# Optimization experiments

Hardware: AMD Instinct MI355X
Metric: run time of the kernel (lower is better)

## Reference

```python
import jax, jax.numpy as jnp
import numpy as np

N, C_DEC, H, W = 16, 512, 32, 32
C_ENC, S, FEATS_IN, N_HEAD = 768, 77, 512, 8
EPS = 1e-5


def setup_inputs() -> dict:
    key = jax.random.key(0)
    ks = jax.random.split(key, 12)
    inp = {
        "input": jax.random.normal(ks[0], (N, C_DEC, H, W), jnp.float32),
        "cond": jax.random.normal(ks[1], (N, FEATS_IN), jnp.float32),
        "enc_hidden": jax.random.normal(ks[2], (N, S, C_ENC), jnp.float32),
        "enc_padding_mask": jax.random.randint(ks[3], (N, S), 0, 2).astype(jnp.float32),
        # AdaGN linear: feats_in -> 2*c_dec (scales, shifts)
        "adagn_w": jax.random.normal(ks[4], (2 * C_DEC, FEATS_IN), jnp.float32) * 0.02,
        "adagn_b": jnp.zeros((2 * C_DEC,), jnp.float32),
        # LayerNorm(c_enc) affine
        "ln_w": jnp.ones((C_ENC,), jnp.float32),
        "ln_b": jnp.zeros((C_ENC,), jnp.float32),
        # 1x1 conv q projection (treated as channel matmul)
        "q_w": jax.random.normal(ks[5], (C_DEC, C_DEC), jnp.float32) * 0.02,
        "q_b": jnp.zeros((C_DEC,), jnp.float32),
        # kv linear: c_enc -> 2*c_dec
        "kv_w": jax.random.normal(ks[6], (2 * C_DEC, C_ENC), jnp.float32) * 0.02,
        "kv_b": jnp.zeros((2 * C_DEC,), jnp.float32),
        # 1x1 conv out projection
        "out_w": jax.random.normal(ks[7], (C_DEC, C_DEC), jnp.float32) * 0.02,
        "out_b": jnp.zeros((C_DEC,), jnp.float32),
    }
    return inp


def reference(input, cond, enc_hidden, enc_padding_mask,
              adagn_w, adagn_b, ln_w, ln_b,
              q_w, q_b, kv_w, kv_b, out_w, out_b):
    n, c, h, w = input.shape
    d = c // N_HEAD

    # --- AdaGN: GroupNorm(1, c, affine=False) then cond-dependent scale/shift ---
    mu = jnp.mean(input, axis=(1, 2, 3), keepdims=True)
    var = jnp.var(input, axis=(1, 2, 3), keepdims=True)
    normed = (input - mu) * jax.lax.rsqrt(var + EPS)
    ss = cond @ adagn_w.T + adagn_b                      # [n, 2c]
    scales, shifts = ss[:, :c], ss[:, c:]
    x = shifts[:, :, None, None] + normed * (scales[:, :, None, None] + 1.0)

    # --- q projection (1x1 conv == per-pixel channel matmul) ---
    q = jnp.einsum('nchw,oc->nohw', x, q_w) + q_b[None, :, None, None]
    q = q.reshape(n, N_HEAD, d, h * w).transpose(0, 1, 3, 2)   # [n, head, hw, d]

    # --- encoder LayerNorm + kv projection ---
    mu_e = jnp.mean(enc_hidden, axis=-1, keepdims=True)
    var_e = jnp.var(enc_hidden, axis=-1, keepdims=True)
    e = (enc_hidden - mu_e) * jax.lax.rsqrt(var_e + EPS) * ln_w + ln_b
    kv = e @ kv_w.T + kv_b                               # [n, S, 2c]
    s = kv.shape[1]
    kv = kv.reshape(n, s, 2 * N_HEAD, d).transpose(0, 2, 1, 3)  # [n, 2*head, S, d]
    k, v = kv[:, :N_HEAD], kv[:, N_HEAD:]

    # --- scaled dot-product attention with additive padding mask ---
    scale = d ** (-0.25)
    att = jnp.einsum('nhqd,nhkd->nhqk', q * scale, k * scale)
    att = att - enc_padding_mask[:, None, None, :] * 10000.0
    att = jax.nn.softmax(att, axis=-1)
    y = jnp.einsum('nhqk,nhkd->nhqd', att, v)            # [n, head, hw, d]
    y = y.transpose(0, 1, 3, 2).reshape(n, c, h, w)

    out = jnp.einsum('nchw,oc->nohw', y, out_w) + out_b[None, :, None, None]
    return input + out
```

## Files before the change

### kernel.cpp

```cpp
#include <hip/hip_runtime.h>
#include <math.h>

typedef unsigned short u16;
typedef __bf16 bf16x8 __attribute__((ext_vector_type(8)));
typedef float f32x4 __attribute__((ext_vector_type(4)));

#define AS1 __attribute__((address_space(1)))
#define AS3 __attribute__((address_space(3)))

#define N_    16
#define C_    512
#define HW_   1024
#define CE_   768
#define S_    77
#define NH_   8
#define D_    64
#define FEATS_ 512
#define EPS_  1e-5f
#define TOK_  (N_ * S_)

#define WS_PSTAT 0
#define WS_QBIAS 1024
#define WSU_BYTE 131072
#define U_QW  0
#define U_OW  262144
#define U_KVW 524288
#define U_EB  1310720
#define U_KVB 2256896
#define U_QT  3518464
#define U_XT  11907072

__device__ __forceinline__ u16 f2bf(float f) {
    unsigned u = __float_as_uint(f);
    return (u16)((u + 0x7FFFu + ((u >> 16) & 1u)) >> 16);
}

__global__ __launch_bounds__(256) void mega1_kernel(const float* __restrict__ inp,
                                                    float* __restrict__ pstats,
                                                    const float* __restrict__ qw,
                                                    const float* __restrict__ ow,
                                                    const float* __restrict__ kvw,
                                                    u16* __restrict__ uq,
                                                    u16* __restrict__ uo,
                                                    u16* __restrict__ ukv,
                                                    const float* __restrict__ enc,
                                                    const float* __restrict__ lnw,
                                                    const float* __restrict__ lnb,
                                                    u16* __restrict__ eb,
                                                    const float* __restrict__ cond,
                                                    const float* __restrict__ agw,
                                                    const float* __restrict__ agb,
                                                    float* __restrict__ ssf) {
    __shared__ __align__(16) float smem[16384];
    int bid = blockIdx.x;
    int tid = threadIdx.x;
    if (bid < 256) {
        int n = bid >> 4, slice = bid & 15;
        const float* base = inp + (size_t)n * C_ * HW_ + slice * (C_ * HW_ / 16);
        float s = 0.f, s2 = 0.f;
        const float4* b4 = (const float4*)base;
        for (int i = tid; i < (C_ * HW_ / 16) / 4; i += 256) {
            float4 v = b4[i];
            s  += v.x + v.y + v.z + v.w;
            s2 += v.x * v.x + v.y * v.y + v.z * v.z + v.w * v.w;
        }
        for (int off = 32; off; off >>= 1) {
            s  += __shfl_down(s, off);
            s2 += __shfl_down(s2, off);
        }
        int wid = tid >> 6, lane = tid & 63;
        if (lane == 0) { smem[wid] = s; smem[4 + wid] = s2; }
        __syncthreads();
        if (tid == 0) {
            pstats[bid * 2]     = smem[0] + smem[1] + smem[2] + smem[3];
            pstats[bid * 2 + 1] = smem[4] + smem[5] + smem[6] + smem[7];
        }
    } else if (bid < 1536) {
        int i = (bid - 256) * 256 + tid;
        const float* s; u16* d; int j;
        if (i < 65536)       { s = qw;  d = uq;  j = i; }
        else if (i < 131072) { s = ow;  d = uo;  j = i - 65536; }
        else                 { s = kvw; d = ukv; j = i - 131072; }
        float4 v = ((const float4*)s)[j];
        ushort4 w;
        w.x = f2bf(v.x); w.y = f2bf(v.y); w.z = f2bf(v.z); w.w = f2bf(v.w);
        ((ushort4*)(d))[j] = w;
    } else if (bid < 2768) {
        int tok = bid - 1536;
        const float* row = enc + (size_t)tok * CE_;
        int t = tid;
        float v0 = row[t], v1 = row[t + 256], v2 = row[t + 512];
        float sum = v0 + v1 + v2;
        float sq  = v0 * v0 + v1 * v1 + v2 * v2;
        for (int off = 32; off; off >>= 1) {
            sum += __shfl_down(sum, off);
            sq  += __shfl_down(sq, off);
        }
        int wid = t >> 6, lane = t & 63;
        if (lane == 0) { smem[wid] = sum; smem[4 + wid] = sq; }
        __syncthreads();
        float tot = smem[0] + smem[1] + smem[2] + smem[3];
        float tsq = smem[4] + smem[5] + smem[6] + smem[7];
        float mu  = tot / CE_;
        float var = tsq / CE_ - mu * mu;
        float rstd = rsqrtf(var + EPS_);
        u16* o = eb + (size_t)tok * CE_;
        o[t]       = f2bf((v0 - mu) * rstd * lnw[t] + lnb[t]);
        o[t + 256] = f2bf((v1 - mu) * rstd * lnw[t + 256] + lnb[t + 256]);
        o[t + 512] = f2bf((v2 - mu) * rstd * lnw[t + 512] + lnb[t + 512]);
    } else {
        float (*wz)[512] = (float(*)[512])smem;
        float (*cz)[512] = (float(*)[512])(smem + 8192);
        int r0 = (bid - 2768) * 16;
        for (int i = tid; i < 2048; i += 256) {
            int row = i >> 7, f4 = i & 127;
            *(float4*)&cz[row][f4 * 4] = ((const float4*)(cond + (size_t)row * 512))[f4];
            *(float4*)&wz[row][f4 * 4] = ((const float4*)(agw + (size_t)(r0 + row) * 512))[f4];
        }
        __syncthreads();
        int n = tid >> 4, r = tid & 15;
        float acc = agb[r0 + r];
        for (int i = 0; i < 128; i++) {
            int j = (r + i) & 127;
            float4 c4 = *(const float4*)&cz[n][j * 4];
            float4 w4 = *(const float4*)&wz[r][j * 4];
            acc += c4.x * w4.x + c4.y * w4.y + c4.z * w4.z + c4.w * w4.w;
        }
        ssf[(size_t)n * 1024 + r0 + r] = acc;
    }
}

__global__ __launch_bounds__(256) void mega2_kernel(const float* __restrict__ inp,
                                                    const float* __restrict__ ssf,
                                                    const float* __restrict__ pstats,
                                                    u16* __restrict__ xT,
                                                    const float* __restrict__ qw,
                                                    const float* __restrict__ qb,
                                                    float* __restrict__ qbias) {
    __shared__ __align__(16) float smem[16384];
    __shared__ float muS[16], rsS[16];
    int bid = blockIdx.x;
    int tid = threadIdx.x;
    float cnt = (float)(C_ * HW_);
    if (bid < 2048) {
        int n = bid >> 7, rem = bid & 127;
        int c0 = (rem >> 4) * 64, h0 = (rem & 15) * 64;
        float s = 0.f, s2 = 0.f;
        for (int k = 0; k < 16; k++) {
            s  += pstats[(n * 16 + k) * 2];
            s2 += pstats[(n * 16 + k) * 2 + 1];
        }
        float mu = s / cnt;
        float rstd = rsqrtf(s2 / cnt - mu * mu + EPS_);
        float (*t)[65] = (float(*)[65])smem;
        int rr = tid >> 4, cc = (tid & 15) * 4;
#pragma unroll
        for (int i = 0; i < 4; i++) {
            int cl = rr + i * 16;
            int c = c0 + cl;
            float a = rstd * (ssf[(size_t)n * 1024 + c] + 1.f);
            float4 v = *(const float4*)(inp + ((size_t)n * C_ + c) * HW_ + h0 + cc);
            t[cl][cc + 0] = v.x * a; t[cl][cc + 1] = v.y * a;
            t[cl][cc + 2] = v.z * a; t[cl][cc + 3] = v.w * a;
        }
        __syncthreads();
#pragma unroll
        for (int i = 0; i < 4; i++) {
            int hl = rr + i * 16;
            ushort4 w;
            w.x = f2bf(t[cc + 0][hl]); w.y = f2bf(t[cc + 1][hl]);
            w.z = f2bf(t[cc + 2][hl]); w.w = f2bf(t[cc + 3][hl]);
            *(ushort4*)(xT + ((size_t)n * HW_ + h0 + hl) * C_ + c0 + cc) = w;
        }
    } else {
        float (*wz)[512] = (float(*)[512])smem;
        float (*cz)[512] = (float(*)[512])(smem + 8192);
        int r0 = (bid - 2048) * 16;
        if (tid < 16) {
            float s = 0.f, s2 = 0.f;
            for (int k = 0; k < 16; k++) {
                s  += pstats[(tid * 16 + k) * 2];
                s2 += pstats[(tid * 16 + k) * 2 + 1];
            }
            float mu = s / cnt;
            muS[tid] = mu;
            rsS[tid] = rsqrtf(s2 / cnt - mu * mu + EPS_);
        }
        __syncthreads();
        for (int i = tid; i < 2048; i += 256) {
            int row = i >> 7, f4 = i & 127;
            float4 sc4 = ((const float4*)(ssf + (size_t)row * 1024))[f4];
            float4 sh4 = ((const float4*)(ssf + (size_t)row * 1024 + 512))[f4];
            float mu = muS[row], rs = rsS[row];
            float4 b;
            b.x = sh4.x - mu * (rs * (sc4.x + 1.f));
            b.y = sh4.y - mu * (rs * (sc4.y + 1.f));
            b.z = sh4.z - mu * (rs * (sc4.z + 1.f));
            b.w = sh4.w - mu * (rs * (sc4.w + 1.f));
            *(float4*)&cz[row][f4 * 4] = b;
            *(float4*)&wz[row][f4 * 4] = ((const float4*)(qw + (size_t)(r0 + row) * 512))[f4];
        }
        __syncthreads();
        int n = tid >> 4, r = tid & 15;
        float acc = qb[r0 + r];
        for (int i = 0; i < 128; i++) {
            int j = (r + i) & 127;
            float4 c4 = *(const float4*)&cz[n][j * 4];
            float4 w4 = *(const float4*)&wz[r][j * 4];
            acc += c4.x * w4.x + c4.y * w4.y + c4.z * w4.z + c4.w * w4.w;
        }
        qbias[(size_t)n * 512 + r0 + r] = acc;
    }
}

__device__ __forceinline__ void gemm_mainloop(const u16* __restrict__ A, int lda, int arow0,
                                              const u16* __restrict__ B, int ldb, int brow0, int brmax,
                                              int K, f32x4 (&acc)[4][4], u16* As, u16* Bs) {
    int tid = threadIdx.x;
    int lane = tid & 63;
    int wm = ((tid >> 6) >> 1) * 64, wn = ((tid >> 6) & 1) * 64;
    int srow = tid >> 3;
    int sw = (tid & 7) ^ (srow & 7);
    int ldsoff = tid * 8;
    for (int kt = 0; kt < K; kt += 64) {
        __syncthreads();
#pragma unroll
        for (int i = 0; i < 4; i++) {
            int ar = arow0 + i * 32 + srow;
            const u16* ga = A + (size_t)ar * lda + kt + sw * 8;
            __builtin_amdgcn_global_load_lds((AS1 void*)ga, (AS3 void*)(As + i * 2048 + ldsoff), 16, 0, 0);
            int br = brow0 + i * 32 + srow; if (br > brmax) br = brmax;
            const u16* gb = B + (size_t)br * ldb + kt + sw * 8;
            __builtin_amdgcn_global_load_lds((AS1 void*)gb, (AS3 void*)(Bs + i * 2048 + ldsoff), 16, 0, 0);
        }
        __syncthreads();
#pragma unroll
        for (int kk = 0; kk < 2; kk++) {
            bf16x8 af[4], bfv[4];
            int ks = kk * 4 + (lane >> 4);
#pragma unroll
            for (int mi = 0; mi < 4; mi++) {
                int r = wm + mi * 16 + (lane & 15);
                af[mi] = *(const bf16x8*)(As + r * 64 + (ks ^ (r & 7)) * 8);
            }
#pragma unroll
            for (int ni = 0; ni < 4; ni++) {
                int r = wn + ni * 16 + (lane & 15);
                bfv[ni] = *(const bf16x8*)(Bs + r * 64 + (ks ^ (r & 7)) * 8);
            }
#pragma unroll
            for (int mi = 0; mi < 4; mi++)
#pragma unroll
                for (int ni = 0; ni < 4; ni++)
                    acc[mi][ni] = __builtin_amdgcn_mfma_f32_16x16x32_bf16(af[mi], bfv[ni], acc[mi][ni], 0, 0, 0);
        }
    }
}

__global__ __launch_bounds__(256) void mega3_kernel(const u16* __restrict__ qwb,
                                                    const u16* __restrict__ xT,
                                                    const float* __restrict__ qbias,
                                                    u16* __restrict__ qt,
                                                    const u16* __restrict__ kvwb,
                                                    const u16* __restrict__ eb,
                                                    const float* __restrict__ kvbias,
                                                    u16* __restrict__ kvo) {
    __shared__ __align__(16) u16 As[128 * 64];
    __shared__ __align__(16) u16 Bs[128 * 64];
    int bid = blockIdx.x;
    int lane = threadIdx.x & 63, wid = threadIdx.x >> 6;
    int wm = (wid >> 1) * 64, wn = (wid & 1) * 64;
    f32x4 acc[4][4];
#pragma unroll
    for (int mi = 0; mi < 4; mi++)
#pragma unroll
        for (int ni = 0; ni < 4; ni++) acc[mi][ni] = 0.f;

    if (bid < 512) {
        int n = bid >> 5, r = bid & 31;
        int brow0 = (r & 7) * 128, arow0 = (r >> 3) * 128;
        gemm_mainloop(qwb, C_, arow0, xT + (size_t)n * HW_ * C_, C_, brow0, HW_ - 1, C_, acc, As, Bs);
        u16* CT = qt + (size_t)n * HW_ * C_;
        const float* qbn = qbias + n * C_;
#pragma unroll
        for (int mi = 0; mi < 4; mi++) {
            int row = arow0 + wm + mi * 16 + ((lane >> 4) << 2);
            float4 b4 = *(const float4*)(qbn + row);
#pragma unroll
            for (int ni = 0; ni < 4; ni++) {
                int col = brow0 + wn + ni * 16 + (lane & 15);
                f32x4 v = acc[mi][ni];
                ushort4 w;
                w.x = f2bf(v.x + b4.x); w.y = f2bf(v.y + b4.y);
                w.z = f2bf(v.z + b4.z); w.w = f2bf(v.w + b4.w);
                *(ushort4*)(CT + (size_t)col * C_ + row) = w;
            }
        }
    } else {
        int t = bid - 512;
        int brow0 = (t % 10) * 128, arow0 = (t / 10) * 128;
        gemm_mainloop(kvwb, CE_, arow0, eb, CE_, brow0, TOK_ - 1, CE_, acc, As, Bs);
#pragma unroll
        for (int mi = 0; mi < 4; mi++) {
            int row = arow0 + wm + mi * 16 + ((lane >> 4) << 2);
            float4 b4 = *(const float4*)(kvbias + row);
#pragma unroll
            for (int ni = 0; ni < 4; ni++) {
                int col = brow0 + wn + ni * 16 + (lane & 15);
                if (col < TOK_) {
                    f32x4 v = acc[mi][ni];
                    ushort4 w;
                    w.x = f2bf(v.x + b4.x); w.y = f2bf(v.y + b4.y);
                    w.z = f2bf(v.z + b4.z); w.w = f2bf(v.w + b4.w);
                    *(ushort4*)(kvo + (size_t)col * 1024 + row) = w;
                }
            }
        }
    }
}

__global__ __launch_bounds__(256) void gemm_out_mfma(const u16* __restrict__ owb,
                                                     const u16* __restrict__ yT,
                                                     const float* __restrict__ ob,
                                                     const float* __restrict__ inp,
                                                     float* __restrict__ outp) {
    __shared__ __align__(16) u16 As[128 * 64];
    __shared__ __align__(16) u16 Bs[128 * 64];
    int n = blockIdx.z;
    int arow0 = blockIdx.y * 128, brow0 = blockIdx.x * 128;
    f32x4 acc[4][4];
#pragma unroll
    for (int mi = 0; mi < 4; mi++)
#pragma unroll
        for (int ni = 0; ni < 4; ni++) acc[mi][ni] = 0.f;
    gemm_mainloop(owb, C_, arow0, yT + (size_t)n * HW_ * C_, C_, brow0, HW_ - 1, C_, acc, As, Bs);
    int lane = threadIdx.x & 63, wid = threadIdx.x >> 6;
    int wm = (wid >> 1) * 64, wn = (wid & 1) * 64;
    float* Co = outp + (size_t)n * C_ * HW_;
    const float* In = inp + (size_t)n * C_ * HW_;
#pragma unroll
    for (int mi = 0; mi < 4; mi++) {
        int row = arow0 + wm + mi * 16 + ((lane >> 4) << 2);
        float4 b4 = *(const float4*)(ob + row);
#pragma unroll
        for (int ni = 0; ni < 4; ni++) {
            int col = brow0 + wn + ni * 16 + (lane & 15);
            f32x4 v = acc[mi][ni];
            size_t i0 = (size_t)row * HW_ + col;
            Co[i0]            = v.x + b4.x + In[i0];
            Co[i0 + HW_]      = v.y + b4.y + In[i0 + HW_];
            Co[i0 + 2 * HW_]  = v.z + b4.z + In[i0 + 2 * HW_];
            Co[i0 + 3 * HW_]  = v.w + b4.w + In[i0 + 3 * HW_];
        }
    }
}

__global__ __launch_bounds__(256) void attn_mfma(const u16* __restrict__ kvb,
                                                 const float* __restrict__ mask,
                                                 const u16* __restrict__ qt,
                                                 u16* __restrict__ yt) {
    int nh = blockIdx.x;
    int n = nh >> 3, h = nh & 7;
    __shared__ __align__(16) u16 Qs[64 * 64];
    __shared__ __align__(16) u16 Ks[80 * 64];
    __shared__ __align__(16) u16 VT[64 * 104];
    __shared__ __align__(16) u16 Ps[64 * 104];
    __shared__ float msk[80];
    int tid = threadIdx.x;
    int lane = tid & 63, w = tid >> 6;
    int g = lane >> 4, l15 = lane & 15;

    const u16* kbase = kvb + (size_t)(n * S_) * 1024 + h * 64;
#pragma unroll
    for (int pass = 0; pass < 3; pass++) {
        int idx = pass * 256 + tid;
        if (idx < 640) {
            int row = idx >> 3, slot = idx & 7;
            int srow = row < S_ ? row : S_ - 1;
            int sw = slot ^ (row & 7);
            __builtin_amdgcn_global_load_lds((AS1 void*)(kbase + (size_t)srow * 1024 + sw * 8),
                                             (AS3 void*)(Ks + idx * 8), 16, 0, 0);
        }
    }
    {
        int d = tid & 63, sg = tid >> 6;
        const u16* vbase = kvb + (size_t)(n * S_) * 1024 + 512 + h * 64 + d;
        for (int s = sg; s < 104; s += 4) {
            u16 v = (s < S_) ? vbase[(size_t)s * 1024] : (u16)0;
            VT[d * 104 + s] = v;
        }
    }
    for (int i = tid; i < 512; i += 256) {
        int r = i >> 3, cp = i & 7;
        *(unsigned*)&Ps[r * 104 + 80 + cp * 2] = 0u;
    }
    if (tid < 80) msk[tid] = (tid < S_) ? mask[n * S_ + tid] * 10000.f : 0.f;

    int qrow = w * 16 + l15;

    for (int qi = 0; qi < 4; qi++) {
        int qb = blockIdx.y * 4 + qi;
        __syncthreads();
        const u16* qbase = qt + ((size_t)(n * HW_ + qb * 64)) * C_ + h * 64;
#pragma unroll
        for (int pass = 0; pass < 2; pass++) {
            int idx = pass * 256 + tid;
            int row = idx >> 3, slot = idx & 7;
            int sw = slot ^ (row & 7);
            __builtin_amdgcn_global_load_lds((AS1 void*)(qbase + (size_t)row * C_ + sw * 8),
                                             (AS3 void*)(Qs + idx * 8), 16, 0, 0);
        }
        __syncthreads();

        bf16x8 qf[2];
#pragma unroll
        for (int kk = 0; kk < 2; kk++) {
            int s8 = kk * 4 + g;
            qf[kk] = *(const bf16x8*)(Qs + qrow * 64 + (s8 ^ (qrow & 7)) * 8);
        }
        f32x4 sc[5];
#pragma unroll
        for (int kb = 0; kb < 5; kb++) {
            sc[kb] = 0.f;
#pragma unroll
            for (int kk = 0; kk < 2; kk++) {
                int r = kb * 16 + l15;
                int s8 = kk * 4 + g;
                bf16x8 kf = *(const bf16x8*)(Ks + r * 64 + (s8 ^ (r & 7)) * 8);
                sc[kb] = __builtin_amdgcn_mfma_f32_16x16x32_bf16(kf, qf[kk], sc[kb], 0, 0, 0);
            }
        }
        float sv[5][4];
        float mx = -3e38f;
#pragma unroll
        for (int kb = 0; kb < 5; kb++)
#pragma unroll
            for (int j = 0; j < 4; j++) {
                int key = kb * 16 + g * 4 + j;
                float s = sc[kb][j] * 0.125f - msk[key];
                sv[kb][j] = s;
                if (key < S_) mx = fmaxf(mx, s);
            }
        mx = fmaxf(mx, __shfl_xor(mx, 16));
        mx = fmaxf(mx, __shfl_xor(mx, 32));
        float sum = 0.f;
        float p[5][4];
#pragma unroll
        for (int kb = 0; kb < 5; kb++)
#pragma unroll
            for (int j = 0; j < 4; j++) {
                int key = kb * 16 + g * 4 + j;
                float pv = (key < S_) ? __expf(sv[kb][j] - mx) : 0.f;
                p[kb][j] = pv;
                sum += pv;
            }
        sum += __shfl_xor(sum, 16);
        sum += __shfl_xor(sum, 32);
        float inv = 1.f / sum;
#pragma unroll
        for (int kb = 0; kb < 5; kb++) {
            unsigned lo = (unsigned)f2bf(p[kb][0] * inv) | ((unsigned)f2bf(p[kb][1] * inv) << 16);
            unsigned hi = (unsigned)f2bf(p[kb][2] * inv) | ((unsigned)f2bf(p[kb][3] * inv) << 16);
            int col = kb * 16 + g * 4;
            *(uint2*)&Ps[qrow * 104 + col] = make_uint2(lo, hi);
        }
        f32x4 ya[4];
#pragma unroll
        for (int mf = 0; mf < 4; mf++) ya[mf] = 0.f;
#pragma unroll
        for (int kk = 0; kk < 3; kk++) {
            int s8 = kk * 4 + g;
            bf16x8 pf = *(const bf16x8*)(Ps + qrow * 104 + s8 * 8);
#pragma unroll
            for (int mf = 0; mf < 4; mf++) {
                bf16x8 vf = *(const bf16x8*)(VT + (mf * 16 + l15) * 104 + s8 * 8);
                ya[mf] = __builtin_amdgcn_mfma_f32_16x16x32_bf16(vf, pf, ya[mf], 0, 0, 0);
            }
        }
        u16* yrow = yt + ((size_t)(n * HW_ + qb * 64 + qrow)) * C_ + h * 64;
#pragma unroll
        for (int mf = 0; mf < 4; mf++) {
            int d0 = mf * 16 + g * 4;
            ushort4 o;
            o.x = f2bf(ya[mf][0]); o.y = f2bf(ya[mf][1]);
            o.z = f2bf(ya[mf][2]); o.w = f2bf(ya[mf][3]);
            *(ushort4*)(yrow + d0) = o;
        }
    }
}

extern "C" void kernel_launch(void* const* d_in, const int* in_sizes, int n_in,
                              void* d_out, int out_size, void* d_ws, size_t ws_size,
                              hipStream_t stream) {
    const float* inp  = (const float*)d_in[0];
    const float* cond = (const float*)d_in[1];
    const float* enc  = (const float*)d_in[2];
    const float* mask = (const float*)d_in[3];
    const float* agw  = (const float*)d_in[4];
    const float* agb  = (const float*)d_in[5];
    const float* lnw  = (const float*)d_in[6];
    const float* lnb  = (const float*)d_in[7];
    const float* qw   = (const float*)d_in[8];
    const float* qb   = (const float*)d_in[9];
    const float* kvw  = (const float*)d_in[10];
    const float* kvb  = (const float*)d_in[11];
    const float* ow   = (const float*)d_in[12];
    const float* ob   = (const float*)d_in[13];
    float* ws  = (float*)d_ws;
    float* out = (float*)d_out;
    u16* wsu = (u16*)((char*)d_ws + WSU_BYTE);
    float* ssf = (float*)(wsu + U_QT);

    mega1_kernel<<<dim3(2832), 256, 0, stream>>>(inp, ws + WS_PSTAT,
                                                 qw, ow, kvw, wsu + U_QW, wsu + U_OW, wsu + U_KVW,
                                                 enc, lnw, lnb, wsu + U_EB,
                                                 cond, agw, agb, ssf);
    mega2_kernel<<<dim3(2080), 256, 0, stream>>>(inp, ssf, ws + WS_PSTAT,
                                                 wsu + U_XT, qw, qb, ws + WS_QBIAS);
    mega3_kernel<<<dim3(592), 256, 0, stream>>>(wsu + U_QW, wsu + U_XT, ws + WS_QBIAS, wsu + U_QT,
                                                wsu + U_KVW, wsu + U_EB, kvb, wsu + U_KVB);

    attn_mfma<<<dim3(N_ * NH_, 4), 256, 0, stream>>>(
        wsu + U_KVB, mask, wsu + U_QT, wsu + U_XT);

    gemm_out_mfma<<<dim3(HW_ / 128, C_ / 128, N_), 256, 0, stream>>>(
        wsu + U_OW, wsu + U_XT, ob, inp, out);
}
```

Before: 102.0 us.

## Fuse Q projection with attention and move KV GEMM into mega2

Moves the KV projection GEMM out of mega3 into extra blocks of mega2. mega3 now computes each Q tile (128 channels = 2 heads × 128 pixels) and keeps it in LDS, then runs the masked softmax attention for those two heads directly, writing Y. This removes the separate attention kernel launch and the round trip of Q through global memory. The cost is higher LDS use per block in mega3 and K/V being reloaded by every Q tile block.

```diff
diff --git a/kernel.cpp b/kernel.cpp
--- a/kernel.cpp
+++ b/kernel.cpp
@@ -27,12 +27,56 @@
 #define U_KVW 524288
 #define U_EB  1310720
 #define U_KVB 2256896
-#define U_QT  3518464
+#define U_YT  3518464
 #define U_XT  11907072
 
 __device__ __forceinline__ u16 f2bf(float f) {
     unsigned u = __float_as_uint(f);
     return (u16)((u + 0x7FFFu + ((u >> 16) & 1u)) >> 16);
+}
+
+__device__ __forceinline__ void gemm_mainloop(const u16* __restrict__ A, int lda, int arow0,
+                                              const u16* __restrict__ B, int ldb, int brow0, int brmax,
+                                              int K, f32x4 (&acc)[4][4], u16* As, u16* Bs) {
+    int tid = threadIdx.x;
+    int lane = tid & 63;
+    int wm = ((tid >> 6) >> 1) * 64, wn = ((tid >> 6) & 1) * 64;
+    int srow = tid >> 3;
+    int sw = (tid & 7) ^ (srow & 7);
+    int ldsoff = tid * 8;
+    for (int kt = 0; kt < K; kt += 64) {
+        __syncthreads();
+#pragma unroll
+        for (int i = 0; i < 4; i++) {
+            int ar = arow0 + i * 32 + srow;
+            const u16* ga = A + (size_t)ar * lda + kt + sw * 8;
+            __builtin_amdgcn_global_load_lds((AS1 void*)ga, (AS3 void*)(As + i * 2048 + ldsoff), 16, 0, 0);
+            int br = brow0 + i * 32 + srow; if (br > brmax) br = brmax;
+            const u16* gb = B + (size_t)br * ldb + kt + sw * 8;
+            __builtin_amdgcn_global_load_lds((AS1 void*)gb, (AS3 void*)(Bs + i * 2048 + ldsoff), 16, 0, 0);
+        }
+        __syncthreads();
+#pragma unroll
+        for (int kk = 0; kk < 2; kk++) {
+            bf16x8 af[4], bfv[4];
+            int ks = kk * 4 + (lane >> 4);
+#pragma unroll
+            for (int mi = 0; mi < 4; mi++) {
+                int r = wm + mi * 16 + (lane & 15);
+                af[mi] = *(const bf16x8*)(As + r * 64 + (ks ^ (r & 7)) * 8);
+            }
+#pragma unroll
+            for (int ni = 0; ni < 4; ni++) {
+                int r = wn + ni * 16 + (lane & 15);
+                bfv[ni] = *(const bf16x8*)(Bs + r * 64 + (ks ^ (r & 7)) * 8);
+            }
+#pragma unroll
+            for (int mi = 0; mi < 4; mi++)
+#pragma unroll
+                for (int ni = 0; ni < 4; ni++)
+                    acc[mi][ni] = __builtin_amdgcn_mfma_f32_16x16x32_bf16(af[mi], bfv[ni], acc[mi][ni], 0, 0, 0);
+        }
+    }
 }
 
 __global__ __launch_bounds__(256) void mega1_kernel(const float* __restrict__ inp,
@@ -136,7 +180,11 @@
                                                     u16* __restrict__ xT,
                                                     const float* __restrict__ qw,
                                                     const float* __restrict__ qb,
-                                                    float* __restrict__ qbias) {
+                                                    float* __restrict__ qbias,
+                                                    const u16* __restrict__ kvwb,
+                                                    const u16* __restrict__ eb,
+                                                    const float* __restrict__ kvbias,
+                                                    u16* __restrict__ kvo) {
     __shared__ __align__(16) float smem[16384];
     __shared__ float muS[16], rsS[16];
     int bid = blockIdx.x;
@@ -172,7 +220,7 @@
             w.z = f2bf(t[cc + 2][hl]); w.w = f2bf(t[cc + 3][hl]);
             *(ushort4*)(xT + ((size_t)n * HW_ + h0 + hl) * C_ + c0 + cc) = w;
         }
-    } else {
+    } else if (bid < 2080) {
         float (*wz)[512] = (float(*)[512])smem;
         float (*cz)[512] = (float(*)[512])(smem + 8192);
         int r0 = (bid - 2048) * 16;
@@ -210,49 +258,35 @@
             acc += c4.x * w4.x + c4.y * w4.y + c4.z * w4.z + c4.w * w4.w;
         }
         qbias[(size_t)n * 512 + r0 + r] = acc;
-    }
-}
-
-__device__ __forceinline__ void gemm_mainloop(const u16* __restrict__ A, int lda, int arow0,
-                                              const u16* __restrict__ B, int ldb, int brow0, int brmax,
-                                              int K, f32x4 (&acc)[4][4], u16* As, u16* Bs) {
-    int tid = threadIdx.x;
-    int lane = tid & 63;
-    int wm = ((tid >> 6) >> 1) * 64, wn = ((tid >> 6) & 1) * 64;
-    int srow = tid >> 3;
-    int sw = (tid & 7) ^ (srow & 7);
-    int ldsoff = tid * 8;
-    for (int kt = 0; kt < K; kt += 64) {
-        __syncthreads();
-#pragma unroll
-        for (int i = 0; i < 4; i++) {
-            int ar = arow0 + i * 32 + srow;
-            const u16* ga = A + (size_t)ar * lda + kt + sw * 8;
-            __builtin_amdgcn_global_load_lds((AS1 void*)ga, (AS3 void*)(As + i * 2048 + ldsoff), 16, 0, 0);
-            int br = brow0 + i * 32 + srow; if (br > brmax) br = brmax;
-            const u16* gb = B + (size_t)br * ldb + kt + sw * 8;
-            __builtin_amdgcn_global_load_lds((AS1 void*)gb, (AS3 void*)(Bs + i * 2048 + ldsoff), 16, 0, 0);
-        }
-        __syncthreads();
-#pragma unroll
-        for (int kk = 0; kk < 2; kk++) {
-            bf16x8 af[4], bfv[4];
-            int ks = kk * 4 + (lane >> 4);
-#pragma unroll
-            for (int mi = 0; mi < 4; mi++) {
-                int r = wm + mi * 16 + (lane & 15);
-                af[mi] = *(const bf16x8*)(As + r * 64 + (ks ^ (r & 7)) * 8);
-            }
+    } else {
+        u16* As = (u16*)smem;
+        u16* Bs = (u16*)smem + 8192;
+        int t = bid - 2080;
+        int brow0 = (t % 10) * 128, arow0 = (t / 10) * 128;
+        f32x4 acc[4][4];
+#pragma unroll
+        for (int mi = 0; mi < 4; mi++)
+#pragma unroll
+            for (int ni = 0; ni < 4; ni++) acc[mi][ni] = 0.f;
+        gemm_mainloop(kvwb, CE_, arow0, eb, CE_, brow0, TOK_ - 1, CE_, acc, As, Bs);
+        int lane = tid & 63, wid = tid >> 6;
+        int wm = (wid >> 1) * 64, wn = (wid & 1) * 64;
+        int g = lane >> 4, l15 = lane & 15;
+#pragma unroll
+        for (int mi = 0; mi < 4; mi++) {
+            int row = arow0 + wm + mi * 16 + (g << 2);
+            float4 b4 = *(const float4*)(kvbias + row);
 #pragma unroll
             for (int ni = 0; ni < 4; ni++) {
-                int r = wn + ni * 16 + (lane & 15);
-                bfv[ni] = *(const bf16x8*)(Bs + r * 64 + (ks ^ (r & 7)) * 8);
-            }
-#pragma unroll
-            for (int mi = 0; mi < 4; mi++)
-#pragma unroll
-                for (int ni = 0; ni < 4; ni++)
-                    acc[mi][ni] = __builtin_amdgcn_mfma_f32_16x16x32_bf16(af[mi], bfv[ni], acc[mi][ni], 0, 0, 0);
+                int col = brow0 + wn + ni * 16 + l15;
+                if (col < TOK_) {
+                    f32x4 v = acc[mi][ni];
+                    ushort4 wv;
+                    wv.x = f2bf(v[0] + b4.x); wv.y = f2bf(v[1] + b4.y);
+                    wv.z = f2bf(v[2] + b4.z); wv.w = f2bf(v[3] + b4.w);
+                    *(ushort4*)(kvo + (size_t)col * 1024 + row) = wv;
+                }
+            }
         }
     }
 }
@@ -260,60 +294,158 @@
 __global__ __launch_bounds__(256) void mega3_kernel(const u16* __restrict__ qwb,
                                                     const u16* __restrict__ xT,
                                                     const float* __restrict__ qbias,
-                                                    u16* __restrict__ qt,
-                                                    const u16* __restrict__ kvwb,
-                                                    const u16* __restrict__ eb,
-                                                    const float* __restrict__ kvbias,
-                                                    u16* __restrict__ kvo) {
-    __shared__ __align__(16) u16 As[128 * 64];
-    __shared__ __align__(16) u16 Bs[128 * 64];
+                                                    const u16* __restrict__ kvo,
+                                                    const float* __restrict__ mask,
+                                                    u16* __restrict__ yt) {
+    __shared__ __align__(16) u16 pool[16384];
+    __shared__ __align__(16) u16 Ks[80 * 64];
+    __shared__ __align__(16) u16 VT[64 * 104];
+    __shared__ __align__(16) u16 Ps[64 * 104];
+    __shared__ float msk[80];
+    u16* As = pool;
+    u16* Bs = pool + 8192;
     int bid = blockIdx.x;
-    int lane = threadIdx.x & 63, wid = threadIdx.x >> 6;
-    int wm = (wid >> 1) * 64, wn = (wid & 1) * 64;
+    int tid = threadIdx.x;
+    int lane = tid & 63, w = tid >> 6;
+    int g = lane >> 4, l15 = lane & 15;
+    int wm = (w >> 1) * 64, wn = (w & 1) * 64;
     f32x4 acc[4][4];
 #pragma unroll
     for (int mi = 0; mi < 4; mi++)
 #pragma unroll
         for (int ni = 0; ni < 4; ni++) acc[mi][ni] = 0.f;
 
-    if (bid < 512) {
-        int n = bid >> 5, r = bid & 31;
-        int brow0 = (r & 7) * 128, arow0 = (r >> 3) * 128;
-        gemm_mainloop(qwb, C_, arow0, xT + (size_t)n * HW_ * C_, C_, brow0, HW_ - 1, C_, acc, As, Bs);
-        u16* CT = qt + (size_t)n * HW_ * C_;
-        const float* qbn = qbias + n * C_;
-#pragma unroll
-        for (int mi = 0; mi < 4; mi++) {
-            int row = arow0 + wm + mi * 16 + ((lane >> 4) << 2);
-            float4 b4 = *(const float4*)(qbn + row);
-#pragma unroll
-            for (int ni = 0; ni < 4; ni++) {
-                int col = brow0 + wn + ni * 16 + (lane & 15);
-                f32x4 v = acc[mi][ni];
-                ushort4 w;
-                w.x = f2bf(v.x + b4.x); w.y = f2bf(v.y + b4.y);
-                w.z = f2bf(v.z + b4.z); w.w = f2bf(v.w + b4.w);
-                *(ushort4*)(CT + (size_t)col * C_ + row) = w;
-            }
-        }
-    } else {
-        int t = bid - 512;
-        int brow0 = (t % 10) * 128, arow0 = (t / 10) * 128;
-        gemm_mainloop(kvwb, CE_, arow0, eb, CE_, brow0, TOK_ - 1, CE_, acc, As, Bs);
-#pragma unroll
-        for (int mi = 0; mi < 4; mi++) {
-            int row = arow0 + wm + mi * 16 + ((lane >> 4) << 2);
-            float4 b4 = *(const float4*)(kvbias + row);
-#pragma unroll
-            for (int ni = 0; ni < 4; ni++) {
-                int col = brow0 + wn + ni * 16 + (lane & 15);
-                if (col < TOK_) {
-                    f32x4 v = acc[mi][ni];
-                    ushort4 w;
-                    w.x = f2bf(v.x + b4.x); w.y = f2bf(v.y + b4.y);
-                    w.z = f2bf(v.z + b4.z); w.w = f2bf(v.w + b4.w);
-                    *(ushort4*)(kvo + (size_t)col * 1024 + row) = w;
+    int n = bid >> 5, r = bid & 31;
+    int brow0 = (r & 7) * 128, arow0 = (r >> 3) * 128;
+    gemm_mainloop(qwb, C_, arow0, xT + (size_t)n * HW_ * C_, C_, brow0, HW_ - 1, C_, acc, As, Bs);
+    __syncthreads();
+
+    const float* qbn = qbias + n * C_;
+#pragma unroll
+    for (int mi = 0; mi < 4; mi++) {
+        int o_loc = wm + mi * 16 + g * 4;
+        float4 b4 = *(const float4*)(qbn + arow0 + o_loc);
+#pragma unroll
+        for (int ni = 0; ni < 4; ni++) {
+            int hw_loc = wn + ni * 16 + l15;
+            f32x4 v = acc[mi][ni];
+            ushort4 wv;
+            wv.x = f2bf(v[0] + b4.x); wv.y = f2bf(v[1] + b4.y);
+            wv.z = f2bf(v[2] + b4.z); wv.w = f2bf(v[3] + b4.w);
+            int dd = o_loc & 63, hsel = o_loc >> 6;
+            int col = hsel * 64 + (((dd >> 3) ^ (hw_loc & 7)) << 3) + (dd & 7);
+            *(ushort4*)&pool[hw_loc * 128 + col] = wv;
+        }
+    }
+    for (int i = tid; i < 512; i += 256) {
+        int rr = i >> 3, cp = i & 7;
+        *(unsigned*)&Ps[rr * 104 + 80 + cp * 2] = 0u;
+    }
+    if (tid < 80) msk[tid] = (tid < S_) ? mask[n * S_ + tid] * 10000.f : 0.f;
+    __syncthreads();
+
+    int h_base = arow0 >> 6;
+    for (int hl = 0; hl < 2; hl++) {
+        int h = h_base + hl;
+        if (hl) __syncthreads();
+        const u16* kbase = kvo + (size_t)(n * S_) * 1024 + h * 64;
+#pragma unroll
+        for (int pass = 0; pass < 3; pass++) {
+            int idx = pass * 256 + tid;
+            if (idx < 640) {
+                int row = idx >> 3, slot = idx & 7;
+                int srow = row < S_ ? row : S_ - 1;
+                int sw = slot ^ (row & 7);
+                __builtin_amdgcn_global_load_lds((AS1 void*)(kbase + (size_t)srow * 1024 + sw * 8),
+                                                 (AS3 void*)(Ks + idx * 8), 16, 0, 0);
+            }
+        }
+        {
+            int d = tid & 63, sg = tid >> 6;
+            const u16* vbase = kvo + (size_t)(n * S_) * 1024 + 512 + h * 64 + d;
+            for (int s = sg; s < 104; s += 4) {
+                u16 v = (s < S_) ? vbase[(size_t)s * 1024] : (u16)0;
+                VT[d * 104 + s] = v;
+            }
+        }
+        __syncthreads();
+
+        for (int qhalf = 0; qhalf < 2; qhalf++) {
+            int qrl = qhalf * 64 + w * 16 + l15;
+            bf16x8 qf[2];
+#pragma unroll
+            for (int kk = 0; kk < 2; kk++) {
+                int s8 = kk * 4 + g;
+                qf[kk] = *(const bf16x8*)(pool + qrl * 128 + hl * 64 + ((s8 ^ (qrl & 7)) << 3));
+            }
+            f32x4 sc[5];
+#pragma unroll
+            for (int kb = 0; kb < 5; kb++) {
+                sc[kb] = 0.f;
+#pragma unroll
+                for (int kk = 0; kk < 2; kk++) {
+                    int rr = kb * 16 + l15;
+                    int s8 = kk * 4 + g;
+                    bf16x8 kf = *(const bf16x8*)(Ks + rr * 64 + ((s8 ^ (rr & 7)) << 3));
+                    sc[kb] = __builtin_amdgcn_mfma_f32_16x16x32_bf16(kf, qf[kk], sc[kb], 0, 0, 0);
                 }
+            }
+            float sv[5][4];
+            float mx = -3e38f;
+#pragma unroll
+            for (int kb = 0; kb < 5; kb++)
+#pragma unroll
+                for (int j = 0; j < 4; j++) {
+                    int key = kb * 16 + g * 4 + j;
+                    float s = sc[kb][j] * 0.125f - msk[key];
+                    sv[kb][j] = s;
+                    if (key < S_) mx = fmaxf(mx, s);
+                }
+            mx = fmaxf(mx, __shfl_xor(mx, 16));
+            mx = fmaxf(mx, __shfl_xor(mx, 32));
+            float sum = 0.f;
+            float p[5][4];
+#pragma unroll
+            for (int kb = 0; kb < 5; kb++)
+#pragma unroll
+                for (int j = 0; j < 4; j++) {
+                    int key = kb * 16 + g * 4 + j;
+                    float pv = (key < S_) ? __expf(sv[kb][j] - mx) : 0.f;
+                    p[kb][j] = pv;
+                    sum += pv;
+                }
+            sum += __shfl_xor(sum, 16);
+            sum += __shfl_xor(sum, 32);
+            float inv = 1.f / sum;
+            int prow = w * 16 + l15;
+#pragma unroll
+            for (int kb = 0; kb < 5; kb++) {
+                unsigned lo = (unsigned)f2bf(p[kb][0] * inv) | ((unsigned)f2bf(p[kb][1] * inv) << 16);
+                unsigned hi = (unsigned)f2bf(p[kb][2] * inv) | ((unsigned)f2bf(p[kb][3] * inv) << 16);
+                int col = kb * 16 + g * 4;
+                *(uint2*)&Ps[prow * 104 + col] = make_uint2(lo, hi);
+            }
+            f32x4 ya[4];
+#pragma unroll
+            for (int mf = 0; mf < 4; mf++) ya[mf] = 0.f;
+#pragma unroll
+            for (int kk = 0; kk < 3; kk++) {
+                int s8 = kk * 4 + g;
+                bf16x8 pf = *(const bf16x8*)(Ps + prow * 104 + s8 * 8);
+#pragma unroll
+                for (int mf = 0; mf < 4; mf++) {
+                    bf16x8 vf = *(const bf16x8*)(VT + (mf * 16 + l15) * 104 + s8 * 8);
+                    ya[mf] = __builtin_amdgcn_mfma_f32_16x16x32_bf16(vf, pf, ya[mf], 0, 0, 0);
+                }
+            }
+            u16* yrow = yt + ((size_t)(n * HW_ + brow0 + qrl)) * C_ + h * 64;
+#pragma unroll
+            for (int mf = 0; mf < 4; mf++) {
+                int d0 = mf * 16 + g * 4;
+                ushort4 o;
+                o.x = f2bf(ya[mf][0]); o.y = f2bf(ya[mf][1]);
+                o.z = f2bf(ya[mf][2]); o.w = f2bf(ya[mf][3]);
+                *(ushort4*)(yrow + d0) = o;
             }
         }
     }
@@ -347,144 +479,10 @@
             int col = brow0 + wn + ni * 16 + (lane & 15);
             f32x4 v = acc[mi][ni];
             size_t i0 = (size_t)row * HW_ + col;
-            Co[i0]            = v.x + b4.x + In[i0];
-            Co[i0 + HW_]      = v.y + b4.y + In[i0 + HW_];
-            Co[i0 + 2 * HW_]  = v.z + b4.z + In[i0 + 2 * HW_];
-            Co[i0 + 3 * HW_]  = v.w + b4.w + In[i0 + 3 * HW_];
-        }
-    }
-}
-
-__global__ __launch_bounds__(256) void attn_mfma(const u16* __restrict__ kvb,
-                                                 const float* __restrict__ mask,
-                                                 const u16* __restrict__ qt,
-                                                 u16* __restrict__ yt) {
-    int nh = blockIdx.x;
-    int n = nh >> 3, h = nh & 7;
-    __shared__ __align__(16) u16 Qs[64 * 64];
-    __shared__ __align__(16) u16 Ks[80 * 64];
-    __shared__ __align__(16) u16 VT[64 * 104];
-    __shared__ __align__(16) u16 Ps[64 * 104];
-    __shared__ float msk[80];
-    int tid = threadIdx.x;
-    int lane = tid & 63, w = tid >> 6;
-    int g = lane >> 4, l15 = lane & 15;
-
-    const u16* kbase = kvb + (size_t)(n * S_) * 1024 + h * 64;
-#pragma unroll
-    for (int pass = 0; pass < 3; pass++) {
-        int idx = pass * 256 + tid;
-        if (idx < 640) {
-            int row = idx >> 3, slot = idx & 7;
-            int srow = row < S_ ? row : S_ - 1;
-            int sw = slot ^ (row & 7);
-            __builtin_amdgcn_global_load_lds((AS1 void*)(kbase + (size_t)srow * 1024 + sw * 8),
-                                             (AS3 void*)(Ks + idx * 8), 16, 0, 0);
-        }
-    }
-    {
-        int d = tid & 63, sg = tid >> 6;
-        const u16* vbase = kvb + (size_t)(n * S_) * 1024 + 512 + h * 64 + d;
-        for (int s = sg; s < 104; s += 4) {
-            u16 v = (s < S_) ? vbase[(size_t)s * 1024] : (u16)0;
-            VT[d * 104 + s] = v;
-        }
-    }
-    for (int i = tid; i < 512; i += 256) {
-        int r = i >> 3, cp = i & 7;
-        *(unsigned*)&Ps[r * 104 + 80 + cp * 2] = 0u;
-    }
-    if (tid < 80) msk[tid] = (tid < S_) ? mask[n * S_ + tid] * 10000.f : 0.f;
-
-    int qrow = w * 16 + l15;
-
-    for (int qi = 0; qi < 4; qi++) {
-        int qb = blockIdx.y * 4 + qi;
-        __syncthreads();
-        const u16* qbase = qt + ((size_t)(n * HW_ + qb * 64)) * C_ + h * 64;
-#pragma unroll
-        for (int pass = 0; pass < 2; pass++) {
-            int idx = pass * 256 + tid;
-            int row = idx >> 3, slot = idx & 7;
-            int sw = slot ^ (row & 7);
-            __builtin_amdgcn_global_load_lds((AS1 void*)(qbase + (size_t)row * C_ + sw * 8),
-                                             (AS3 void*)(Qs + idx * 8), 16, 0, 0);
-        }
-        __syncthreads();
-
-        bf16x8 qf[2];
-#pragma unroll
-        for (int kk = 0; kk < 2; kk++) {
-            int s8 = kk * 4 + g;
-            qf[kk] = *(const bf16x8*)(Qs + qrow * 64 + (s8 ^ (qrow & 7)) * 8);
-        }
-        f32x4 sc[5];
-#pragma unroll
-        for (int kb = 0; kb < 5; kb++) {
-            sc[kb] = 0.f;
-#pragma unroll
-            for (int kk = 0; kk < 2; kk++) {
-                int r = kb * 16 + l15;
-                int s8 = kk * 4 + g;
-                bf16x8 kf = *(const bf16x8*)(Ks + r * 64 + (s8 ^ (r & 7)) * 8);
-                sc[kb] = __builtin_amdgcn_mfma_f32_16x16x32_bf16(kf, qf[kk], sc[kb], 0, 0, 0);
-            }
-        }
-        float sv[5][4];
-        float mx = -3e38f;
-#pragma unroll
-        for (int kb = 0; kb < 5; kb++)
-#pragma unroll
-            for (int j = 0; j < 4; j++) {
-                int key = kb * 16 + g * 4 + j;
-                float s = sc[kb][j] * 0.125f - msk[key];
-                sv[kb][j] = s;
-                if (key < S_) mx = fmaxf(mx, s);
-            }
-        mx = fmaxf(mx, __shfl_xor(mx, 16));
-        mx = fmaxf(mx, __shfl_xor(mx, 32));
-        float sum = 0.f;
-        float p[5][4];
-#pragma unroll
-        for (int kb = 0; kb < 5; kb++)
-#pragma unroll
-            for (int j = 0; j < 4; j++) {
-                int key = kb * 16 + g * 4 + j;
-                float pv = (key < S_) ? __expf(sv[kb][j] - mx) : 0.f;
-                p[kb][j] = pv;
-                sum += pv;
-            }
-        sum += __shfl_xor(sum, 16);
-        sum += __shfl_xor(sum, 32);
-        float inv = 1.f / sum;
-#pragma unroll
-        for (int kb = 0; kb < 5; kb++) {
-            unsigned lo = (unsigned)f2bf(p[kb][0] * inv) | ((unsigned)f2bf(p[kb][1] * inv) << 16);
-            unsigned hi = (unsigned)f2bf(p[kb][2] * inv) | ((unsigned)f2bf(p[kb][3] * inv) << 16);
-            int col = kb * 16 + g * 4;
-            *(uint2*)&Ps[qrow * 104 + col] = make_uint2(lo, hi);
-        }
-        f32x4 ya[4];
-#pragma unroll
-        for (int mf = 0; mf < 4; mf++) ya[mf] = 0.f;
-#pragma unroll
-        for (int kk = 0; kk < 3; kk++) {
-            int s8 = kk * 4 + g;
-            bf16x8 pf = *(const bf16x8*)(Ps + qrow * 104 + s8 * 8);
-#pragma unroll
-            for (int mf = 0; mf < 4; mf++) {
-                bf16x8 vf = *(const bf16x8*)(VT + (mf * 16 + l15) * 104 + s8 * 8);
-                ya[mf] = __builtin_amdgcn_mfma_f32_16x16x32_bf16(vf, pf, ya[mf], 0, 0, 0);
-            }
-        }
-        u16* yrow = yt + ((size_t)(n * HW_ + qb * 64 + qrow)) * C_ + h * 64;
-#pragma unroll
-        for (int mf = 0; mf < 4; mf++) {
-            int d0 = mf * 16 + g * 4;
-            ushort4 o;
-            o.x = f2bf(ya[mf][0]); o.y = f2bf(ya[mf][1]);
-            o.z = f2bf(ya[mf][2]); o.w = f2bf(ya[mf][3]);
-            *(ushort4*)(yrow + d0) = o;
+            Co[i0]            = v[0] + b4.x + In[i0];
+            Co[i0 + HW_]      = v[1] + b4.y + In[i0 + HW_];
+            Co[i0 + 2 * HW_]  = v[2] + b4.z + In[i0 + 2 * HW_];
+            Co[i0 + 3 * HW_]  = v[3] + b4.w + In[i0 + 3 * HW_];
         }
     }
 }
@@ -509,20 +507,18 @@
     float* ws  = (float*)d_ws;
     float* out = (float*)d_out;
     u16* wsu = (u16*)((char*)d_ws + WSU_BYTE);
-    float* ssf = (float*)(wsu + U_QT);
+    float* ssf = (float*)(wsu + U_YT);
 
     mega1_kernel<<<dim3(2832), 256, 0, stream>>>(inp, ws + WS_PSTAT,
                                                  qw, ow, kvw, wsu + U_QW, wsu + U_OW, wsu + U_KVW,
                                                  enc, lnw, lnb, wsu + U_EB,
                                                  cond, agw, agb, ssf);
-    mega2_kernel<<<dim3(2080), 256, 0, stream>>>(inp, ssf, ws + WS_PSTAT,
-                                                 wsu + U_XT, qw, qb, ws + WS_QBIAS);
-    mega3_kernel<<<dim3(592), 256, 0, stream>>>(wsu + U_QW, wsu + U_XT, ws + WS_QBIAS, wsu + U_QT,
-                                                wsu + U_KVW, wsu + U_EB, kvb, wsu + U_KVB);
-
-    attn_mfma<<<dim3(N_ * NH_, 4), 256, 0, stream>>>(
-        wsu + U_KVB, mask, wsu + U_QT, wsu + U_XT);
+    mega2_kernel<<<dim3(2160), 256, 0, stream>>>(inp, ssf, ws + WS_PSTAT,
+                                                 wsu + U_XT, qw, qb, ws + WS_QBIAS,
+                                                 wsu + U_KVW, wsu + U_EB, kvb, wsu + U_KVB);
+    mega3_kernel<<<dim3(512), 256, 0, stream>>>(wsu + U_QW, wsu + U_XT, ws + WS_QBIAS,
+                                                wsu + U_KVB, mask, wsu + U_YT);
 
     gemm_out_mfma<<<dim3(HW_ / 128, C_ / 128, N_), 256, 0, stream>>>(
-        wsu + U_OW, wsu + U_XT, ob, inp, out);
-}
+        wsu + U_OW, wsu + U_YT, ob, inp, out);
+}
```

After: 100.6 us. About the same (-1.4%).
